# Performance work log

Measured on AMD Instinct MI355X. Metric: run time of the kernel, lower is better.

Reference implementation:

```python
import jax, jax.numpy as jnp
import numpy as np

# hydroDL 2-layer custom LSTM cell; ngrid must equal hiddenSize (see layer-2 [B,B] matmul)
NT, NGRID, NX, NY, H = 365, 512, 16, 1, 512


def _linear_params(key, out_d, in_d):
    # torch.nn.Linear default init: U(-1/sqrt(in), 1/sqrt(in))
    s = 1.0 / np.sqrt(in_d)
    kw, kb = jax.random.split(key)
    W = jax.random.uniform(kw, (out_d, in_d), minval=-s, maxval=s, dtype=jnp.float32)
    b = jax.random.uniform(kb, (out_d,), minval=-s, maxval=s, dtype=jnp.float32)
    return W, b


def setup_inputs() -> dict:
    key = jax.random.key(0)
    ks = jax.random.split(key, 7)
    x = jax.random.normal(ks[0], (NT, NGRID, NX), dtype=jnp.float32)
    W_in, b_in = _linear_params(ks[1], H, NX)          # linearIn (doReLU=True)
    W_ih0, b_ih0 = _linear_params(ks[2], 4 * H, H)     # w_ih[0] (inputSize=H after relu)
    W_hh0, b_hh0 = _linear_params(ks[3], 4 * H, H)     # w_hh[0]
    W_ih1, b_ih1 = _linear_params(ks[4], 4 * H, H)     # w_ih[1]
    W_hh1, b_hh1 = _linear_params(ks[5], 4 * H, H)     # w_hh[1]
    W_out, b_out = _linear_params(ks[6], NY, H)        # linearOut
    return dict(x=x, W_in=W_in, b_in=b_in,
                W_ih0=W_ih0, b_ih0=b_ih0, W_hh0=W_hh0, b_hh0=b_hh0,
                W_ih1=W_ih1, b_ih1=b_ih1, W_hh1=W_hh1, b_hh1=b_hh1,
                W_out=W_out, b_out=b_out)


def reference(x, W_in, b_in, W_ih0, b_ih0, W_hh0, b_hh0,
              W_ih1, b_ih1, W_hh1, b_hh1, W_out, b_out):
    nt = x.shape[0]
    # doReLU branch: batch the input projection across all timesteps
    x0 = jax.nn.relu(jnp.einsum('tbn,hn->tbh', x, W_in) + b_in)  # [NT, B, H]
    h0 = jnp.zeros((NGRID, H), dtype=x.dtype)
    c0 = jnp.zeros((NGRID, H), dtype=x.dtype)
    sg = jax.lax.stop_gradient

    def step(carry, xt):
        ht, ct, s = carry
        # ---- layer 0: standard LSTM cell (no dropout: eval mode) ----
        g0 = xt @ W_ih0.T + b_ih0 + ht @ W_hh0.T + b_hh0          # [B, 4H]
        i0, f0, cg0, o0 = jnp.split(g0, 4, axis=1)
        i0 = jax.nn.sigmoid(i0)
        f0 = jax.nn.sigmoid(f0)
        cg0 = jnp.tanh(cg0)
        o0 = jax.nn.sigmoid(o0)
        ct = f0 * ct + i0 * cg0
        ht = o0 * jnp.tanh(ct)
        # ---- layer 1: raw gates mixed with layer-0 gates via [B,B] matmuls ----
        # (original does this in detached numpy, so everything here is stop_gradient)
        g1 = xt @ W_ih1.T + b_ih1 + ht @ W_hh1.T + b_hh1          # [B, 4H]
        ir, fr, cr, orr = jnp.split(g1, 4, axis=1)
        si = sg(i0) @ sg(ir).T     # [B, B]
        sf = sg(f0) @ sg(fr).T
        sc = sg(cg0) @ sg(cr).T
        so = sg(o0) @ sg(orr).T
        i1 = jax.nn.sigmoid(si)
        f1 = jax.nn.sigmoid(sf)
        c1 = jnp.tanh(sc)
        o1 = jax.nn.sigmoid(so)
        s = s + (jnp.var(si) + jnp.var(sf) + jnp.var(sc) + jnp.var(so)) / 4.0
        # [B,B] elementwise with [B,H]; valid because B == H
        ct = f1 * ct + i1 * c1
        ht = o1 * jnp.tanh(ct)
        return (ht, ct, s), ht

    (_, _, s), outs = jax.lax.scan(step, (h0, c0, jnp.float32(0.0)), x0)
    out = jnp.einsum('tbh,yh->tby', outs, W_out) + b_out          # [NT, B, NY]
    norm = s / nt
    return (out, norm)
```

## Files before the change

### kernel.cpp

```cpp
#include <hip/hip_runtime.h>

#define NT 365
#define NB 512
#define NX4 16

typedef __attribute__((ext_vector_type(8))) short bf16x8;
typedef __attribute__((ext_vector_type(4))) float f32x4;
typedef __attribute__((ext_vector_type(4))) unsigned int u32x4;
typedef unsigned short u16;
typedef unsigned int u32;

static constexpr size_t WB_OFF  = 0;
static constexpr size_t B0_OFF  = WB_OFF + 4ull * 2048 * 512 * 2;
static constexpr size_t B1_OFF  = B0_OFF + 2048 * 4;
static constexpr size_t X0_OFF  = B1_OFF + 2048 * 4;
static constexpr size_t HT_OFF  = X0_OFF + 512 * 512 * 2;
static constexpr size_t HT0_OFF = HT_OFF + 512 * 512 * 2;
static constexpr size_t G0_OFF  = HT0_OFF + 512 * 512 * 2;
static constexpr size_t G1_OFF  = G0_OFF + 4ull * 512 * 512 * 2;
static constexpr size_t CT_OFF  = G1_OFF + 4ull * 512 * 512 * 2;
static constexpr size_t VSP_OFF = CT_OFF + 512ull * 512 * 4;
static constexpr size_t NRM_OFF = VSP_OFF + 256ull * 8 * 368 * 4;

__device__ __forceinline__ u16 f2bf(float f) {
  u32 u = __builtin_bit_cast(u32, f);
  return (u16)((u + 0x7fffu + ((u >> 16) & 1u)) >> 16);
}
__device__ __forceinline__ float bf2f(u16 h) {
  u32 u = ((u32)h) << 16;
  return __builtin_bit_cast(float, u);
}
__device__ __forceinline__ float sigf(float x) { return 1.0f / (1.0f + __expf(-x)); }
__device__ __forceinline__ float tanha(float x) { return 1.0f - 2.0f / (__expf(2.0f * x) + 1.0f); }

__global__ __launch_bounds__(1024) void prep_k(
    const float* __restrict__ xg, const float* __restrict__ Win, const float* __restrict__ bin,
    const float* __restrict__ Wih0, const float* __restrict__ bih0,
    const float* __restrict__ Whh0, const float* __restrict__ bhh0,
    const float* __restrict__ Wih1, const float* __restrict__ bih1,
    const float* __restrict__ Whh1, const float* __restrict__ bhh1,
    const float* __restrict__ bout, float* __restrict__ out, char* __restrict__ ws) {
  u16* wb = (u16*)(ws + WB_OFF);
  float* b0 = (float*)(ws + B0_OFF);
  float* b1 = (float*)(ws + B1_OFF);
  u16* x0b = (u16*)(ws + X0_OFF);
  u16* htb = (u16*)(ws + HT_OFF);
  float* ctb = (float*)(ws + CT_OFF);
  const int gtid = blockIdx.x * 1024 + threadIdx.x;

  const float* srcs[4] = {Wih0, Whh0, Wih1, Whh1};
  #pragma unroll
  for (int mm = 0; mm < 4; ++mm) {
    const float4* s4 = (const float4*)srcs[mm];
    float4 v = s4[gtid];
    ushort4 o;
    o.x = f2bf(v.x); o.y = f2bf(v.y); o.z = f2bf(v.z); o.w = f2bf(v.w);
    ((ushort4*)(wb + (size_t)mm * 2048 * 512))[gtid] = o;
  }
  if (gtid < 2048) { b0[gtid] = bih0[gtid] + bhh0[gtid]; b1[gtid] = bih1[gtid] + bhh1[gtid]; }
  if (gtid < 131072) ((u32*)htb)[gtid] = 0u;
  ctb[gtid] = 0.0f;
  {
    int b = gtid >> 9, h = gtid & 511;
    const float* xr = xg + (size_t)b * NX4;
    const float* wr = Win + (size_t)h * NX4;
    float a = bin[h];
    #pragma unroll
    for (int j = 0; j < 16; ++j) a += wr[j] * xr[j];
    x0b[gtid] = f2bf(fmaxf(a, 0.0f));
  }
  {
    float bo = bout[0];
    for (int j = gtid; j < NT * NB; j += 262144) out[j] = bo;
  }
}

__global__ __launch_bounds__(1024) void p1_k(char* __restrict__ ws) {
  __shared__ __align__(16) char lraw[65536];
  u16* gFu = (u16*)lraw;
  u16* wb = (u16*)(ws + WB_OFF);
  float* b0 = (float*)(ws + B0_OFF);
  u16* x0b = (u16*)(ws + X0_OFF);
  u16* htb = (u16*)(ws + HT_OFF);
  u16* ht0b = (u16*)(ws + HT0_OFF);
  u16* g0b = (u16*)(ws + G0_OFF);
  float* ctb = (float*)(ws + CT_OFF);

  const int tid = threadIdx.x, gid = blockIdx.x;
  const int r = gid >> 4, c = gid & 15;
  const int rbase = r * 32, cbase = c * 32;
  const int w = tid >> 6, lane = tid & 63, l15 = lane & 15, kg = lane >> 4;
  const int g = w >> 2, m = (w >> 1) & 1, n = w & 1;
  const int urow = tid >> 5, ucol = tid & 31;
  const int ub = rbase + urow, uh = cbase + ucol;
  const int arow = m * 16 + l15, abase = arow << 11, axor = (arow & 7) << 4;
  const u16* Wl0 = wb + (size_t)(g * 512 + cbase + n * 16 + l15) * 512;
  const float bias0l = b0[g * 512 + cbase + n * 16 + l15];

  #pragma unroll
  for (int p = 0; p < 4; ++p) {
    int ch = p * 1024 + tid;
    int row = ch >> 7, cc = ch & 127;
    const u16* sp = (cc < 64) ? x0b + (size_t)(rbase + row) * 512 + cc * 8
                              : htb + (size_t)(rbase + row) * 512 + (cc - 64) * 8;
    u32x4 v = *(const u32x4*)sp;
    *(u32x4*)&lraw[(row << 11) | ((cc << 4) ^ ((row & 7) << 4))] = v;
  }
  __syncthreads();
  f32x4 acc = {0.f, 0.f, 0.f, 0.f};
  {
    const u16* W0 = Wl0;
    const u16* W1 = Wl0 + 2048ull * 512;
    #pragma unroll
    for (int ks = 0; ks < 16; ++ks) {
      int kk = ks * 32 + kg * 8;
      bf16x8 a = *(const bf16x8*)&lraw[abase | (((kk >> 3) << 4) ^ axor)];
      bf16x8 q = *(const bf16x8*)(W0 + kk);
      acc = __builtin_amdgcn_mfma_f32_16x16x32_bf16(a, q, acc, 0, 0, 0);
    }
    #pragma unroll
    for (int ks = 0; ks < 16; ++ks) {
      int kk = ks * 32 + kg * 8;
      bf16x8 a = *(const bf16x8*)&lraw[abase | (((64 + (kk >> 3)) << 4) ^ axor)];
      bf16x8 q = *(const bf16x8*)(W1 + kk);
      acc = __builtin_amdgcn_mfma_f32_16x16x32_bf16(a, q, acc, 0, 0, 0);
    }
  }
  __syncthreads();
  #pragma unroll
  for (int q = 0; q < 4; ++q) {
    float v = acc[q] + bias0l;
    float a = (g == 2) ? tanha(v) : sigf(v);
    gFu[g * 1280 + (m * 16 + kg * 4 + q) * 40 + n * 16 + l15] = f2bf(a);
  }
  __syncthreads();
  {
    u16 gi = gFu[0 * 1280 + urow * 40 + ucol];
    u16 gf = gFu[1 * 1280 + urow * 40 + ucol];
    u16 gc = gFu[2 * 1280 + urow * 40 + ucol];
    u16 go = gFu[3 * 1280 + urow * 40 + ucol];
    float i0 = bf2f(gi), f0 = bf2f(gf), c0 = bf2f(gc), o0 = bf2f(go);
    size_t eo = (size_t)ub * 512 + uh;
    float ctv = ctb[eo];
    ctv = f0 * ctv + i0 * c0;
    float h0v = o0 * tanha(ctv);
    ctb[eo] = ctv;
    ht0b[eo] = f2bf(h0v);
    g0b[0 * 262144 + eo] = gi;
    g0b[1 * 262144 + eo] = gf;
    g0b[2 * 262144 + eo] = gc;
    g0b[3 * 262144 + eo] = go;
  }
}

__global__ __launch_bounds__(1024) void p2_k(char* __restrict__ ws) {
  __shared__ __align__(16) char lraw[65536];
  u16* wb = (u16*)(ws + WB_OFF);
  float* b1 = (float*)(ws + B1_OFF);
  u16* x0b = (u16*)(ws + X0_OFF);
  u16* ht0b = (u16*)(ws + HT0_OFF);
  u16* g1b = (u16*)(ws + G1_OFF);

  const int tid = threadIdx.x, gid = blockIdx.x;
  const int r = gid >> 4, c = gid & 15;
  const int rbase = r * 32, cbase = c * 32;
  const int w = tid >> 6, lane = tid & 63, l15 = lane & 15, kg = lane >> 4;
  const int g = w >> 2, m = (w >> 1) & 1, n = w & 1;
  const int arow = m * 16 + l15, abase = arow << 11, axor = (arow & 7) << 4;
  const u16* Wl0 = wb + (size_t)(g * 512 + cbase + n * 16 + l15) * 512;
  const float bias1l = b1[g * 512 + cbase + n * 16 + l15];

  #pragma unroll
  for (int p = 0; p < 4; ++p) {
    int ch = p * 1024 + tid;
    int row = ch >> 7, cc = ch & 127;
    const u16* sp = (cc < 64) ? x0b + (size_t)(rbase + row) * 512 + cc * 8
                              : ht0b + (size_t)(rbase + row) * 512 + (cc - 64) * 8;
    u32x4 v = *(const u32x4*)sp;
    *(u32x4*)&lraw[(row << 11) | ((cc << 4) ^ ((row & 7) << 4))] = v;
  }
  __syncthreads();
  f32x4 acc = {0.f, 0.f, 0.f, 0.f};
  {
    const u16* W0 = Wl0 + 2ull * 2048 * 512;
    const u16* W1 = Wl0 + 3ull * 2048 * 512;
    #pragma unroll
    for (int ks = 0; ks < 16; ++ks) {
      int kk = ks * 32 + kg * 8;
      bf16x8 a = *(const bf16x8*)&lraw[abase | (((kk >> 3) << 4) ^ axor)];
      bf16x8 q = *(const bf16x8*)(W0 + kk);
      acc = __builtin_amdgcn_mfma_f32_16x16x32_bf16(a, q, acc, 0, 0, 0);
    }
    #pragma unroll
    for (int ks = 0; ks < 16; ++ks) {
      int kk = ks * 32 + kg * 8;
      bf16x8 a = *(const bf16x8*)&lraw[abase | (((64 + (kk >> 3)) << 4) ^ axor)];
      bf16x8 q = *(const bf16x8*)(W1 + kk);
      acc = __builtin_amdgcn_mfma_f32_16x16x32_bf16(a, q, acc, 0, 0, 0);
    }
  }
  #pragma unroll
  for (int q = 0; q < 4; ++q) {
    int b_ = rbase + m * 16 + kg * 4 + q;
    g1b[(size_t)g * 262144 + (size_t)b_ * 512 + cbase + n * 16 + l15] = f2bf(acc[q] + bias1l);
  }
}

__global__ __launch_bounds__(1024) void p3_k(
    char* __restrict__ ws, const float* __restrict__ xg, const float* __restrict__ Win,
    const float* __restrict__ bin, const float* __restrict__ Wout,
    float* __restrict__ out, int t) {
  __shared__ u16 gFu[5120];
  __shared__ float sv[32];
  u16* x0b = (u16*)(ws + X0_OFF);
  u16* htb = (u16*)(ws + HT_OFF);
  u16* g0b = (u16*)(ws + G0_OFF);
  u16* g1b = (u16*)(ws + G1_OFF);
  float* ctb = (float*)(ws + CT_OFF);
  float* vspb = (float*)(ws + VSP_OFF);

  const int tid = threadIdx.x, gid = blockIdx.x;
  const int r = gid >> 4, c = gid & 15;
  const int rbase = r * 32, cbase = c * 32;
  const int w = tid >> 6, lane = tid & 63, l15 = lane & 15, kg = lane >> 4;
  const int g = w >> 2, m = (w >> 1) & 1, n = w & 1;
  const int urow = tid >> 5, ucol = tid & 31;
  const int ub = rbase + urow, uh = cbase + ucol;

  {
    f32x4 acc = {0.f, 0.f, 0.f, 0.f};
    const u16* As = g0b + (size_t)g * 262144 + (size_t)(rbase + m * 16 + l15) * 512;
    const u16* Bs = g1b + (size_t)g * 262144 + (size_t)(cbase + n * 16 + l15) * 512;
    #pragma unroll
    for (int ks = 0; ks < 16; ++ks) {
      int kk = ks * 32 + kg * 8;
      bf16x8 a = *(const bf16x8*)(As + kk);
      bf16x8 q = *(const bf16x8*)(Bs + kk);
      acc = __builtin_amdgcn_mfma_f32_16x16x32_bf16(a, q, acc, 0, 0, 0);
    }
    float s1 = acc[0] + acc[1] + acc[2] + acc[3];
    float s2 = acc[0] * acc[0] + acc[1] * acc[1] + acc[2] * acc[2] + acc[3] * acc[3];
    #pragma unroll
    for (int off = 32; off > 0; off >>= 1) { s1 += __shfl_xor(s1, off); s2 += __shfl_xor(s2, off); }
    if (lane == 0) { sv[w * 2] = s1; sv[w * 2 + 1] = s2; }
    #pragma unroll
    for (int q = 0; q < 4; ++q)
      gFu[g * 1280 + (m * 16 + kg * 4 + q) * 40 + n * 16 + l15] = f2bf(acc[q]);
  }
  __syncthreads();
  {
    float i1 = sigf(bf2f(gFu[0 * 1280 + urow * 40 + ucol]));
    float f1 = sigf(bf2f(gFu[1 * 1280 + urow * 40 + ucol]));
    float c1 = tanha(bf2f(gFu[2 * 1280 + urow * 40 + ucol]));
    float o1 = sigf(bf2f(gFu[3 * 1280 + urow * 40 + ucol]));
    size_t eo = (size_t)ub * 512 + uh;
    float ctv = ctb[eo];
    ctv = f1 * ctv + i1 * c1;
    float hv = o1 * tanha(ctv);
    ctb[eo] = ctv;
    htb[eo] = f2bf(hv);
    float op = hv * Wout[uh];
    op += __shfl_down(op, 16, 32);
    op += __shfl_down(op, 8, 32);
    op += __shfl_down(op, 4, 32);
    op += __shfl_down(op, 2, 32);
    op += __shfl_down(op, 1, 32);
    if ((tid & 31) == 0) atomicAdd(out + (size_t)t * NB + ub, op);
    if (tid < 8) {
      int gg = tid >> 1, part = tid & 1;
      float val = sv[(gg * 4 + 0) * 2 + part] + sv[(gg * 4 + 1) * 2 + part] +
                  sv[(gg * 4 + 2) * 2 + part] + sv[(gg * 4 + 3) * 2 + part];
      vspb[((size_t)gid * 8 + tid) * 368 + t] = val;
    }
    if (t + 1 < NT) {
      const float* xr = xg + ((size_t)(t + 1) * NB + ub) * NX4;
      const float* wr = Win + (size_t)uh * NX4;
      float a = bin[uh];
      #pragma unroll
      for (int j = 0; j < 16; ++j) a += wr[j] * xr[j];
      x0b[eo] = f2bf(fmaxf(a, 0.0f));
    }
  }
}

__global__ __launch_bounds__(256) void var_k(char* __restrict__ ws) {
  __shared__ float sred[8];
  float* vspb = (float*)(ws + VSP_OFF);
  float* normp = (float*)(ws + NRM_OFF);
  const int tt = blockIdx.x;
  const int tid = threadIdx.x;
  const int s = tid >> 5, jb = tid & 31;
  float v = 0.0f;
  for (int j = jb; j < 256; j += 32) v += vspb[((size_t)j * 8 + s) * 368 + tt];
  #pragma unroll
  for (int off = 16; off > 0; off >>= 1) v += __shfl_xor(v, off, 32);
  if (jb == 0) sred[s] = v;
  __syncthreads();
  if (tid == 0) {
    const float invN = 1.0f / 262144.0f;
    float var4 = 0.0f;
    #pragma unroll
    for (int gg = 0; gg < 4; ++gg) {
      float sum = sred[gg * 2 + 0];
      float sq  = sred[gg * 2 + 1];
      float mean = sum * invN;
      var4 += sq * invN - mean * mean;
    }
    normp[tt] = var4 * 0.25f;
  }
}

__global__ __launch_bounds__(512) void final_k(char* __restrict__ ws, float* __restrict__ out) {
  __shared__ float red[8];
  float* normp = (float*)(ws + NRM_OFF);
  const int tid = threadIdx.x;
  float s = (tid < NT) ? normp[tid] : 0.0f;
  #pragma unroll
  for (int off = 32; off > 0; off >>= 1) s += __shfl_xor(s, off);
  if ((tid & 63) == 0) red[tid >> 6] = s;
  __syncthreads();
  if (tid == 0) {
    float tot = 0.0f;
    #pragma unroll
    for (int j = 0; j < 8; ++j) tot += red[j];
    out[NT * NB] = tot / (float)NT;
  }
}

extern "C" void kernel_launch(void* const* d_in, const int* in_sizes, int n_in,
                              void* d_out, int out_size, void* d_ws, size_t ws_size,
                              hipStream_t stream) {
  const float* xg = (const float*)d_in[0];
  const float* Win = (const float*)d_in[1];
  const float* bin = (const float*)d_in[2];
  const float* Wih0 = (const float*)d_in[3];
  const float* bih0 = (const float*)d_in[4];
  const float* Whh0 = (const float*)d_in[5];
  const float* bhh0 = (const float*)d_in[6];
  const float* Wih1 = (const float*)d_in[7];
  const float* bih1 = (const float*)d_in[8];
  const float* Whh1 = (const float*)d_in[9];
  const float* bhh1 = (const float*)d_in[10];
  const float* Wout = (const float*)d_in[11];
  const float* bout = (const float*)d_in[12];
  float* out = (float*)d_out;
  char* ws = (char*)d_ws;

  hipLaunchKernelGGL(prep_k, dim3(256), dim3(1024), 0, stream,
                     xg, Win, bin, Wih0, bih0, Whh0, bhh0, Wih1, bih1, Whh1, bhh1,
                     bout, out, ws);
  for (int t = 0; t < NT; ++t) {
    hipLaunchKernelGGL(p1_k, dim3(256), dim3(1024), 0, stream, ws);
    hipLaunchKernelGGL(p2_k, dim3(256), dim3(1024), 0, stream, ws);
    hipLaunchKernelGGL(p3_k, dim3(256), dim3(1024), 0, stream, ws, xg, Win, bin, Wout, out, t);
  }
  hipLaunchKernelGGL(var_k, dim3(365), dim3(256), 0, stream, ws);
  hipLaunchKernelGGL(final_k, dim3(1), dim3(512), 0, stream, ws, out);
}
```

Baseline: 21.20 ms.

## Precompute input-gate projections off the recurrence path and overlap them with layer-1 mixing

The x0 @ W_ih contributions for both layers, with biases folded in, are now computed as fp32 tiles by extra blocks appended to the p3 launch for the next timestep. This removes the input half of the K dimension from the serial p1/p2 GEMMs, so each of those only multiplies by W_hh over K=512 and drops its LDS staging. The next-step x0 computation moves into p2h. The cost is extra fp32 workspace traffic and larger p3 grids. The new path runs only when the workspace is large enough, otherwise the old path is kept as a fallback.

```diff
diff --git a/kernel.cpp b/kernel.cpp
--- a/kernel.cpp
+++ b/kernel.cpp
@@ -21,6 +21,9 @@
 static constexpr size_t CT_OFF  = G1_OFF + 4ull * 512 * 512 * 2;
 static constexpr size_t VSP_OFF = CT_OFF + 512ull * 512 * 4;
 static constexpr size_t NRM_OFF = VSP_OFF + 256ull * 8 * 368 * 4;
+static constexpr size_t G0X_OFF = (NRM_OFF + 368 * 4 + 255) & ~255ull;
+static constexpr size_t G1X_OFF = G0X_OFF + 4ull * 512 * 512 * 4;
+static constexpr size_t WS_NEED = G1X_OFF + 4ull * 512 * 512 * 4;
 
 __device__ __forceinline__ u16 f2bf(float f) {
   u32 u = __builtin_bit_cast(u32, f);
@@ -75,16 +78,47 @@
   }
 }
 
-__global__ __launch_bounds__(1024) void p1_k(char* __restrict__ ws) {
-  __shared__ __align__(16) char lraw[65536];
-  u16* gFu = (u16*)lraw;
+__device__ __forceinline__ void xproj_tile(char* __restrict__ ws, int M, int j, int tid) {
   u16* wb = (u16*)(ws + WB_OFF);
-  float* b0 = (float*)(ws + B0_OFF);
-  u16* x0b = (u16*)(ws + X0_OFF);
-  u16* htb = (u16*)(ws + HT_OFF);
+  const float* bias = (const float*)(ws + (M ? B1_OFF : B0_OFF));
+  const u16* x0b = (const u16*)(ws + X0_OFF);
+  float* gx = (float*)(ws + (M ? G1X_OFF : G0X_OFF));
+  const u16* W = wb + (size_t)(M ? 2 : 0) * 2048 * 512;
+  const int r = j >> 4, c = j & 15;
+  const int rbase = r * 32, cbase = c * 32;
+  const int w = tid >> 6, lane = tid & 63, l15 = lane & 15, kg = lane >> 4;
+  const int g = w >> 2, m = (w >> 1) & 1, n = w & 1;
+  const int wrow = g * 512 + cbase + n * 16 + l15;
+  const u16* Wr = W + (size_t)wrow * 512;
+  const u16* Ar = x0b + (size_t)(rbase + m * 16 + l15) * 512;
+  f32x4 acc = {0.f, 0.f, 0.f, 0.f};
+  const float bb = bias[wrow];
+  #pragma unroll
+  for (int ks = 0; ks < 16; ++ks) {
+    int kk = ks * 32 + kg * 8;
+    bf16x8 a = *(const bf16x8*)(Ar + kk);
+    bf16x8 q = *(const bf16x8*)(Wr + kk);
+    acc = __builtin_amdgcn_mfma_f32_16x16x32_bf16(a, q, acc, 0, 0, 0);
+  }
+  #pragma unroll
+  for (int q = 0; q < 4; ++q) {
+    int row = rbase + m * 16 + kg * 4 + q;
+    gx[(size_t)g * 262144 + (size_t)row * 512 + cbase + n * 16 + l15] = acc[q] + bb;
+  }
+}
+
+__global__ __launch_bounds__(1024) void xproj0_k(char* __restrict__ ws) {
+  xproj_tile(ws, blockIdx.x >> 8, blockIdx.x & 255, threadIdx.x);
+}
+
+__global__ __launch_bounds__(1024) void p1h_k(char* __restrict__ ws) {
+  __shared__ u16 gFu[5120];
+  u16* wb = (u16*)(ws + WB_OFF);
+  const u16* htb = (const u16*)(ws + HT_OFF);
   u16* ht0b = (u16*)(ws + HT0_OFF);
   u16* g0b = (u16*)(ws + G0_OFF);
   float* ctb = (float*)(ws + CT_OFF);
+  const float* g0x = (const float*)(ws + G0X_OFF);
 
   const int tid = threadIdx.x, gid = blockIdx.x;
   const int r = gid >> 4, c = gid & 15;
@@ -93,43 +127,25 @@
   const int g = w >> 2, m = (w >> 1) & 1, n = w & 1;
   const int urow = tid >> 5, ucol = tid & 31;
   const int ub = rbase + urow, uh = cbase + ucol;
-  const int arow = m * 16 + l15, abase = arow << 11, axor = (arow & 7) << 4;
-  const u16* Wl0 = wb + (size_t)(g * 512 + cbase + n * 16 + l15) * 512;
-  const float bias0l = b0[g * 512 + cbase + n * 16 + l15];
-
-  #pragma unroll
-  for (int p = 0; p < 4; ++p) {
-    int ch = p * 1024 + tid;
-    int row = ch >> 7, cc = ch & 127;
-    const u16* sp = (cc < 64) ? x0b + (size_t)(rbase + row) * 512 + cc * 8
-                              : htb + (size_t)(rbase + row) * 512 + (cc - 64) * 8;
-    u32x4 v = *(const u32x4*)sp;
-    *(u32x4*)&lraw[(row << 11) | ((cc << 4) ^ ((row & 7) << 4))] = v;
-  }
-  __syncthreads();
-  f32x4 acc = {0.f, 0.f, 0.f, 0.f};
-  {
-    const u16* W0 = Wl0;
-    const u16* W1 = Wl0 + 2048ull * 512;
-    #pragma unroll
-    for (int ks = 0; ks < 16; ++ks) {
-      int kk = ks * 32 + kg * 8;
-      bf16x8 a = *(const bf16x8*)&lraw[abase | (((kk >> 3) << 4) ^ axor)];
-      bf16x8 q = *(const bf16x8*)(W0 + kk);
-      acc = __builtin_amdgcn_mfma_f32_16x16x32_bf16(a, q, acc, 0, 0, 0);
-    }
-    #pragma unroll
-    for (int ks = 0; ks < 16; ++ks) {
-      int kk = ks * 32 + kg * 8;
-      bf16x8 a = *(const bf16x8*)&lraw[abase | (((64 + (kk >> 3)) << 4) ^ axor)];
-      bf16x8 q = *(const bf16x8*)(W1 + kk);
-      acc = __builtin_amdgcn_mfma_f32_16x16x32_bf16(a, q, acc, 0, 0, 0);
-    }
-  }
-  __syncthreads();
+
+  f32x4 acc;
+  #pragma unroll
+  for (int q = 0; q < 4; ++q)
+    acc[q] = g0x[(size_t)g * 262144 + (size_t)(rbase + m * 16 + kg * 4 + q) * 512 + cbase + n * 16 + l15];
+  {
+    const u16* Wr = wb + 1ull * 2048 * 512 + (size_t)(g * 512 + cbase + n * 16 + l15) * 512;
+    const u16* Ar = htb + (size_t)(rbase + m * 16 + l15) * 512;
+    #pragma unroll
+    for (int ks = 0; ks < 16; ++ks) {
+      int kk = ks * 32 + kg * 8;
+      bf16x8 a = *(const bf16x8*)(Ar + kk);
+      bf16x8 q = *(const bf16x8*)(Wr + kk);
+      acc = __builtin_amdgcn_mfma_f32_16x16x32_bf16(a, q, acc, 0, 0, 0);
+    }
+  }
   #pragma unroll
   for (int q = 0; q < 4; ++q) {
-    float v = acc[q] + bias0l;
+    float v = acc[q];
     float a = (g == 2) ? tanha(v) : sigf(v);
     gFu[g * 1280 + (m * 16 + kg * 4 + q) * 40 + n * 16 + l15] = f2bf(a);
   }
@@ -153,73 +169,68 @@
   }
 }
 
-__global__ __launch_bounds__(1024) void p2_k(char* __restrict__ ws) {
-  __shared__ __align__(16) char lraw[65536];
+__global__ __launch_bounds__(1024) void p2h_k(
+    char* __restrict__ ws, const float* __restrict__ xg, const float* __restrict__ Win,
+    const float* __restrict__ bin, int t) {
   u16* wb = (u16*)(ws + WB_OFF);
-  float* b1 = (float*)(ws + B1_OFF);
   u16* x0b = (u16*)(ws + X0_OFF);
-  u16* ht0b = (u16*)(ws + HT0_OFF);
+  const u16* ht0b = (const u16*)(ws + HT0_OFF);
   u16* g1b = (u16*)(ws + G1_OFF);
+  const float* g1x = (const float*)(ws + G1X_OFF);
 
   const int tid = threadIdx.x, gid = blockIdx.x;
   const int r = gid >> 4, c = gid & 15;
   const int rbase = r * 32, cbase = c * 32;
   const int w = tid >> 6, lane = tid & 63, l15 = lane & 15, kg = lane >> 4;
   const int g = w >> 2, m = (w >> 1) & 1, n = w & 1;
-  const int arow = m * 16 + l15, abase = arow << 11, axor = (arow & 7) << 4;
-  const u16* Wl0 = wb + (size_t)(g * 512 + cbase + n * 16 + l15) * 512;
-  const float bias1l = b1[g * 512 + cbase + n * 16 + l15];
-
-  #pragma unroll
-  for (int p = 0; p < 4; ++p) {
-    int ch = p * 1024 + tid;
-    int row = ch >> 7, cc = ch & 127;
-    const u16* sp = (cc < 64) ? x0b + (size_t)(rbase + row) * 512 + cc * 8
-                              : ht0b + (size_t)(rbase + row) * 512 + (cc - 64) * 8;
-    u32x4 v = *(const u32x4*)sp;
-    *(u32x4*)&lraw[(row << 11) | ((cc << 4) ^ ((row & 7) << 4))] = v;
-  }
-  __syncthreads();
-  f32x4 acc = {0.f, 0.f, 0.f, 0.f};
-  {
-    const u16* W0 = Wl0 + 2ull * 2048 * 512;
-    const u16* W1 = Wl0 + 3ull * 2048 * 512;
-    #pragma unroll
-    for (int ks = 0; ks < 16; ++ks) {
-      int kk = ks * 32 + kg * 8;
-      bf16x8 a = *(const bf16x8*)&lraw[abase | (((kk >> 3) << 4) ^ axor)];
-      bf16x8 q = *(const bf16x8*)(W0 + kk);
-      acc = __builtin_amdgcn_mfma_f32_16x16x32_bf16(a, q, acc, 0, 0, 0);
-    }
-    #pragma unroll
-    for (int ks = 0; ks < 16; ++ks) {
-      int kk = ks * 32 + kg * 8;
-      bf16x8 a = *(const bf16x8*)&lraw[abase | (((64 + (kk >> 3)) << 4) ^ axor)];
-      bf16x8 q = *(const bf16x8*)(W1 + kk);
+  const int urow = tid >> 5, ucol = tid & 31;
+  const int ub = rbase + urow, uh = cbase + ucol;
+
+  f32x4 acc;
+  #pragma unroll
+  for (int q = 0; q < 4; ++q)
+    acc[q] = g1x[(size_t)g * 262144 + (size_t)(rbase + m * 16 + kg * 4 + q) * 512 + cbase + n * 16 + l15];
+  {
+    const u16* Wr = wb + 3ull * 2048 * 512 + (size_t)(g * 512 + cbase + n * 16 + l15) * 512;
+    const u16* Ar = ht0b + (size_t)(rbase + m * 16 + l15) * 512;
+    #pragma unroll
+    for (int ks = 0; ks < 16; ++ks) {
+      int kk = ks * 32 + kg * 8;
+      bf16x8 a = *(const bf16x8*)(Ar + kk);
+      bf16x8 q = *(const bf16x8*)(Wr + kk);
       acc = __builtin_amdgcn_mfma_f32_16x16x32_bf16(a, q, acc, 0, 0, 0);
     }
   }
   #pragma unroll
   for (int q = 0; q < 4; ++q) {
     int b_ = rbase + m * 16 + kg * 4 + q;
-    g1b[(size_t)g * 262144 + (size_t)b_ * 512 + cbase + n * 16 + l15] = f2bf(acc[q] + bias1l);
-  }
-}
-
-__global__ __launch_bounds__(1024) void p3_k(
-    char* __restrict__ ws, const float* __restrict__ xg, const float* __restrict__ Win,
-    const float* __restrict__ bin, const float* __restrict__ Wout,
-    float* __restrict__ out, int t) {
+    g1b[(size_t)g * 262144 + (size_t)b_ * 512 + cbase + n * 16 + l15] = f2bf(acc[q]);
+  }
+  if (t + 1 < NT) {
+    const float* xr = xg + ((size_t)(t + 1) * NB + ub) * NX4;
+    const float* wr = Win + (size_t)uh * NX4;
+    float a = bin[uh];
+    #pragma unroll
+    for (int j = 0; j < 16; ++j) a += wr[j] * xr[j];
+    x0b[(size_t)ub * 512 + uh] = f2bf(fmaxf(a, 0.0f));
+  }
+}
+
+__global__ __launch_bounds__(1024) void p3x_k(
+    char* __restrict__ ws, const float* __restrict__ Wout, float* __restrict__ out, int t) {
+  const int tid = threadIdx.x, gid = blockIdx.x;
+  if (gid >= 256) {
+    if (t + 1 < NT) { int jj = gid - 256; xproj_tile(ws, jj >> 8, jj & 255, tid); }
+    return;
+  }
   __shared__ u16 gFu[5120];
   __shared__ float sv[32];
-  u16* x0b = (u16*)(ws + X0_OFF);
   u16* htb = (u16*)(ws + HT_OFF);
-  u16* g0b = (u16*)(ws + G0_OFF);
-  u16* g1b = (u16*)(ws + G1_OFF);
+  const u16* g0b = (const u16*)(ws + G0_OFF);
+  const u16* g1b = (const u16*)(ws + G1_OFF);
   float* ctb = (float*)(ws + CT_OFF);
   float* vspb = (float*)(ws + VSP_OFF);
 
-  const int tid = threadIdx.x, gid = blockIdx.x;
   const int r = gid >> 4, c = gid & 15;
   const int rbase = r * 32, cbase = c * 32;
   const int w = tid >> 6, lane = tid & 63, l15 = lane & 15, kg = lane >> 4;
@@ -272,6 +283,206 @@
                   sv[(gg * 4 + 2) * 2 + part] + sv[(gg * 4 + 3) * 2 + part];
       vspb[((size_t)gid * 8 + tid) * 368 + t] = val;
     }
+  }
+}
+
+__global__ __launch_bounds__(1024) void p1_k(char* __restrict__ ws) {
+  __shared__ __align__(16) char lraw[65536];
+  u16* gFu = (u16*)lraw;
+  u16* wb = (u16*)(ws + WB_OFF);
+  float* b0 = (float*)(ws + B0_OFF);
+  u16* x0b = (u16*)(ws + X0_OFF);
+  u16* htb = (u16*)(ws + HT_OFF);
+  u16* ht0b = (u16*)(ws + HT0_OFF);
+  u16* g0b = (u16*)(ws + G0_OFF);
+  float* ctb = (float*)(ws + CT_OFF);
+
+  const int tid = threadIdx.x, gid = blockIdx.x;
+  const int r = gid >> 4, c = gid & 15;
+  const int rbase = r * 32, cbase = c * 32;
+  const int w = tid >> 6, lane = tid & 63, l15 = lane & 15, kg = lane >> 4;
+  const int g = w >> 2, m = (w >> 1) & 1, n = w & 1;
+  const int urow = tid >> 5, ucol = tid & 31;
+  const int ub = rbase + urow, uh = cbase + ucol;
+  const int arow = m * 16 + l15, abase = arow << 11, axor = (arow & 7) << 4;
+  const u16* Wl0 = wb + (size_t)(g * 512 + cbase + n * 16 + l15) * 512;
+  const float bias0l = b0[g * 512 + cbase + n * 16 + l15];
+
+  #pragma unroll
+  for (int p = 0; p < 4; ++p) {
+    int ch = p * 1024 + tid;
+    int row = ch >> 7, cc = ch & 127;
+    const u16* sp = (cc < 64) ? x0b + (size_t)(rbase + row) * 512 + cc * 8
+                              : htb + (size_t)(rbase + row) * 512 + (cc - 64) * 8;
+    u32x4 v = *(const u32x4*)sp;
+    *(u32x4*)&lraw[(row << 11) | ((cc << 4) ^ ((row & 7) << 4))] = v;
+  }
+  __syncthreads();
+  f32x4 acc = {0.f, 0.f, 0.f, 0.f};
+  {
+    const u16* W0 = Wl0;
+    const u16* W1 = Wl0 + 2048ull * 512;
+    #pragma unroll
+    for (int ks = 0; ks < 16; ++ks) {
+      int kk = ks * 32 + kg * 8;
+      bf16x8 a = *(const bf16x8*)&lraw[abase | (((kk >> 3) << 4) ^ axor)];
+      bf16x8 q = *(const bf16x8*)(W0 + kk);
+      acc = __builtin_amdgcn_mfma_f32_16x16x32_bf16(a, q, acc, 0, 0, 0);
+    }
+    #pragma unroll
+    for (int ks = 0; ks < 16; ++ks) {
+      int kk = ks * 32 + kg * 8;
+      bf16x8 a = *(const bf16x8*)&lraw[abase | (((64 + (kk >> 3)) << 4) ^ axor)];
+      bf16x8 q = *(const bf16x8*)(W1 + kk);
+      acc = __builtin_amdgcn_mfma_f32_16x16x32_bf16(a, q, acc, 0, 0, 0);
+    }
+  }
+  __syncthreads();
+  #pragma unroll
+  for (int q = 0; q < 4; ++q) {
+    float v = acc[q] + bias0l;
+    float a = (g == 2) ? tanha(v) : sigf(v);
+    gFu[g * 1280 + (m * 16 + kg * 4 + q) * 40 + n * 16 + l15] = f2bf(a);
+  }
+  __syncthreads();
+  {
+    u16 gi = gFu[0 * 1280 + urow * 40 + ucol];
+    u16 gf = gFu[1 * 1280 + urow * 40 + ucol];
+    u16 gc = gFu[2 * 1280 + urow * 40 + ucol];
+    u16 go = gFu[3 * 1280 + urow * 40 + ucol];
+    float i0 = bf2f(gi), f0 = bf2f(gf), c0 = bf2f(gc), o0 = bf2f(go);
+    size_t eo = (size_t)ub * 512 + uh;
+    float ctv = ctb[eo];
+    ctv = f0 * ctv + i0 * c0;
+    float h0v = o0 * tanha(ctv);
+    ctb[eo] = ctv;
+    ht0b[eo] = f2bf(h0v);
+    g0b[0 * 262144 + eo] = gi;
+    g0b[1 * 262144 + eo] = gf;
+    g0b[2 * 262144 + eo] = gc;
+    g0b[3 * 262144 + eo] = go;
+  }
+}
+
+__global__ __launch_bounds__(1024) void p2_k(char* __restrict__ ws) {
+  __shared__ __align__(16) char lraw[65536];
+  u16* wb = (u16*)(ws + WB_OFF);
+  float* b1 = (float*)(ws + B1_OFF);
+  u16* x0b = (u16*)(ws + X0_OFF);
+  u16* ht0b = (u16*)(ws + HT0_OFF);
+  u16* g1b = (u16*)(ws + G1_OFF);
+
+  const int tid = threadIdx.x, gid = blockIdx.x;
+  const int r = gid >> 4, c = gid & 15;
+  const int rbase = r * 32, cbase = c * 32;
+  const int w = tid >> 6, lane = tid & 63, l15 = lane & 15, kg = lane >> 4;
+  const int g = w >> 2, m = (w >> 1) & 1, n = w & 1;
+  const int arow = m * 16 + l15, abase = arow << 11, axor = (arow & 7) << 4;
+  const u16* Wl0 = wb + (size_t)(g * 512 + cbase + n * 16 + l15) * 512;
+  const float bias1l = b1[g * 512 + cbase + n * 16 + l15];
+
+  #pragma unroll
+  for (int p = 0; p < 4; ++p) {
+    int ch = p * 1024 + tid;
+    int row = ch >> 7, cc = ch & 127;
+    const u16* sp = (cc < 64) ? x0b + (size_t)(rbase + row) * 512 + cc * 8
+                              : ht0b + (size_t)(rbase + row) * 512 + (cc - 64) * 8;
+    u32x4 v = *(const u32x4*)sp;
+    *(u32x4*)&lraw[(row << 11) | ((cc << 4) ^ ((row & 7) << 4))] = v;
+  }
+  __syncthreads();
+  f32x4 acc = {0.f, 0.f, 0.f, 0.f};
+  {
+    const u16* W0 = Wl0 + 2ull * 2048 * 512;
+    const u16* W1 = Wl0 + 3ull * 2048 * 512;
+    #pragma unroll
+    for (int ks = 0; ks < 16; ++ks) {
+      int kk = ks * 32 + kg * 8;
+      bf16x8 a = *(const bf16x8*)&lraw[abase | (((kk >> 3) << 4) ^ axor)];
+      bf16x8 q = *(const bf16x8*)(W0 + kk);
+      acc = __builtin_amdgcn_mfma_f32_16x16x32_bf16(a, q, acc, 0, 0, 0);
+    }
+    #pragma unroll
+    for (int ks = 0; ks < 16; ++ks) {
+      int kk = ks * 32 + kg * 8;
+      bf16x8 a = *(const bf16x8*)&lraw[abase | (((64 + (kk >> 3)) << 4) ^ axor)];
+      bf16x8 q = *(const bf16x8*)(W1 + kk);
+      acc = __builtin_amdgcn_mfma_f32_16x16x32_bf16(a, q, acc, 0, 0, 0);
+    }
+  }
+  #pragma unroll
+  for (int q = 0; q < 4; ++q) {
+    int b_ = rbase + m * 16 + kg * 4 + q;
+    g1b[(size_t)g * 262144 + (size_t)b_ * 512 + cbase + n * 16 + l15] = f2bf(acc[q] + bias1l);
+  }
+}
+
+__global__ __launch_bounds__(1024) void p3_k(
+    char* __restrict__ ws, const float* __restrict__ xg, const float* __restrict__ Win,
+    const float* __restrict__ bin, const float* __restrict__ Wout,
+    float* __restrict__ out, int t) {
+  __shared__ u16 gFu[5120];
+  __shared__ float sv[32];
+  u16* x0b = (u16*)(ws + X0_OFF);
+  u16* htb = (u16*)(ws + HT_OFF);
+  u16* g0b = (u16*)(ws + G0_OFF);
+  u16* g1b = (u16*)(ws + G1_OFF);
+  float* ctb = (float*)(ws + CT_OFF);
+  float* vspb = (float*)(ws + VSP_OFF);
+
+  const int tid = threadIdx.x, gid = blockIdx.x;
+  const int r = gid >> 4, c = gid & 15;
+  const int rbase = r * 32, cbase = c * 32;
+  const int w = tid >> 6, lane = tid & 63, l15 = lane & 15, kg = lane >> 4;
+  const int g = w >> 2, m = (w >> 1) & 1, n = w & 1;
+  const int urow = tid >> 5, ucol = tid & 31;
+  const int ub = rbase + urow, uh = cbase + ucol;
+
+  {
+    f32x4 acc = {0.f, 0.f, 0.f, 0.f};
+    const u16* As = g0b + (size_t)g * 262144 + (size_t)(rbase + m * 16 + l15) * 512;
+    const u16* Bs = g1b + (size_t)g * 262144 + (size_t)(cbase + n * 16 + l15) * 512;
+    #pragma unroll
+    for (int ks = 0; ks < 16; ++ks) {
+      int kk = ks * 32 + kg * 8;
+      bf16x8 a = *(const bf16x8*)(As + kk);
+      bf16x8 q = *(const bf16x8*)(Bs + kk);
+      acc = __builtin_amdgcn_mfma_f32_16x16x32_bf16(a, q, acc, 0, 0, 0);
+    }
+    float s1 = acc[0] + acc[1] + acc[2] + acc[3];
+    float s2 = acc[0] * acc[0] + acc[1] * acc[1] + acc[2] * acc[2] + acc[3] * acc[3];
+    #pragma unroll
+    for (int off = 32; off > 0; off >>= 1) { s1 += __shfl_xor(s1, off); s2 += __shfl_xor(s2, off); }
+    if (lane == 0) { sv[w * 2] = s1; sv[w * 2 + 1] = s2; }
+    #pragma unroll
+    for (int q = 0; q < 4; ++q)
+      gFu[g * 1280 + (m * 16 + kg * 4 + q) * 40 + n * 16 + l15] = f2bf(acc[q]);
+  }
+  __syncthreads();
+  {
+    float i1 = sigf(bf2f(gFu[0 * 1280 + urow * 40 + ucol]));
+    float f1 = sigf(bf2f(gFu[1 * 1280 + urow * 40 + ucol]));
+    float c1 = tanha(bf2f(gFu[2 * 1280 + urow * 40 + ucol]));
+    float o1 = sigf(bf2f(gFu[3 * 1280 + urow * 40 + ucol]));
+    size_t eo = (size_t)ub * 512 + uh;
+    float ctv = ctb[eo];
+    ctv = f1 * ctv + i1 * c1;
+    float hv = o1 * tanha(ctv);
+    ctb[eo] = ctv;
+    htb[eo] = f2bf(hv);
+    float op = hv * Wout[uh];
+    op += __shfl_down(op, 16, 32);
+    op += __shfl_down(op, 8, 32);
+    op += __shfl_down(op, 4, 32);
+    op += __shfl_down(op, 2, 32);
+    op += __shfl_down(op, 1, 32);
+    if ((tid & 31) == 0) atomicAdd(out + (size_t)t * NB + ub, op);
+    if (tid < 8) {
+      int gg = tid >> 1, part = tid & 1;
+      float val = sv[(gg * 4 + 0) * 2 + part] + sv[(gg * 4 + 1) * 2 + part] +
+                  sv[(gg * 4 + 2) * 2 + part] + sv[(gg * 4 + 3) * 2 + part];
+      vspb[((size_t)gid * 8 + tid) * 368 + t] = val;
+    }
     if (t + 1 < NT) {
       const float* xr = xg + ((size_t)(t + 1) * NB + ub) * NX4;
       const float* wr = Win + (size_t)uh * NX4;
@@ -349,10 +560,19 @@
   hipLaunchKernelGGL(prep_k, dim3(256), dim3(1024), 0, stream,
                      xg, Win, bin, Wih0, bih0, Whh0, bhh0, Wih1, bih1, Whh1, bhh1,
                      bout, out, ws);
-  for (int t = 0; t < NT; ++t) {
-    hipLaunchKernelGGL(p1_k, dim3(256), dim3(1024), 0, stream, ws);
-    hipLaunchKernelGGL(p2_k, dim3(256), dim3(1024), 0, stream, ws);
-    hipLaunchKernelGGL(p3_k, dim3(256), dim3(1024), 0, stream, ws, xg, Win, bin, Wout, out, t);
+  if (ws_size >= WS_NEED) {
+    hipLaunchKernelGGL(xproj0_k, dim3(512), dim3(1024), 0, stream, ws);
+    for (int t = 0; t < NT; ++t) {
+      hipLaunchKernelGGL(p1h_k, dim3(256), dim3(1024), 0, stream, ws);
+      hipLaunchKernelGGL(p2h_k, dim3(256), dim3(1024), 0, stream, ws, xg, Win, bin, t);
+      hipLaunchKernelGGL(p3x_k, dim3(768), dim3(1024), 0, stream, ws, Wout, out, t);
+    }
+  } else {
+    for (int t = 0; t < NT; ++t) {
+      hipLaunchKernelGGL(p1_k, dim3(256), dim3(1024), 0, stream, ws);
+      hipLaunchKernelGGL(p2_k, dim3(256), dim3(1024), 0, stream, ws);
+      hipLaunchKernelGGL(p3_k, dim3(256), dim3(1024), 0, stream, ws, xg, Win, bin, Wout, out, t);
+    }
   }
   hipLaunchKernelGGL(var_k, dim3(365), dim3(256), 0, stream, ws);
   hipLaunchKernelGGL(final_k, dim3(1), dim3(512), 0, stream, ws, out);
```

Measured after the change: 30.22 ms. 1.43x slower.
